# Kernel tuning notes

Measured on AMD Instinct MI355X. Metric: run time of the kernel, lower is better.

The kernel has to match this reference:

```python
import jax, jax.numpy as jnp
import numpy as np
import math

B, S, D, H, FF = 32, 577, 768, 12, 3072
Dh = D // H
EPS = 1e-5


def layer_norm(x, w, b):
    mu = jnp.mean(x, axis=-1, keepdims=True)
    var = jnp.mean(jnp.square(x - mu), axis=-1, keepdims=True)
    return (x - mu) * jax.lax.rsqrt(var + EPS) * w + b


def setup_inputs() -> dict:
    key = jax.random.key(0)
    ks = jax.random.split(key, 12)
    s = 0.02
    return {
        "x": jax.random.normal(ks[0], (B, S, D), dtype=jnp.float32),
        "ln1_w": jnp.ones((D,), jnp.float32),
        "ln1_b": jnp.zeros((D,), jnp.float32),
        # stacked per-head Q/K/V projections (head order matches torch concat order)
        "Wq": jax.random.normal(ks[1], (H, D, Dh), jnp.float32) * s,
        "bq": jnp.zeros((H, Dh), jnp.float32),
        "Wk": jax.random.normal(ks[2], (H, D, Dh), jnp.float32) * s,
        "bk": jnp.zeros((H, Dh), jnp.float32),
        "Wv": jax.random.normal(ks[3], (H, D, Dh), jnp.float32) * s,
        "bv": jnp.zeros((H, Dh), jnp.float32),
        "Wo": jax.random.normal(ks[4], (D, D), jnp.float32) * s,
        "bo": jnp.zeros((D,), jnp.float32),
        "ln2_w": jnp.ones((D,), jnp.float32),
        "ln2_b": jnp.zeros((D,), jnp.float32),
        "W1": jax.random.normal(ks[5], (D, FF), jnp.float32) * s,
        "b1": jnp.zeros((FF,), jnp.float32),
        "W2": jax.random.normal(ks[6], (FF, D), jnp.float32) * s,
        "b2": jnp.zeros((D,), jnp.float32),
    }


def reference(x, ln1_w, ln1_b, Wq, bq, Wk, bk, Wv, bv, Wo, bo, ln2_w, ln2_b, W1, b1, W2, b2):
    # pre-norm attention
    h = layer_norm(x, ln1_w, ln1_b)  # [B,S,D]
    q = jnp.einsum('bsd,hde->bhse', h, Wq) + bq[:, None, :]
    k = jnp.einsum('bsd,hde->bhse', h, Wk) + bk[:, None, :]
    v = jnp.einsum('bsd,hde->bhse', h, Wv) + bv[:, None, :]
    scores = jnp.einsum('bhse,bhte->bhst', q, k) / math.sqrt(Dh)
    probs = jax.nn.softmax(scores, axis=-1)
    ctx = jnp.einsum('bhst,bhte->bhse', probs, v)  # [B,H,S,Dh]
    ctx = ctx.transpose(0, 2, 1, 3).reshape(B, S, H * Dh)  # concat heads
    attn_out = ctx @ Wo + bo
    x = x + attn_out
    # pre-norm MLP (exact GELU, as nn.GELU default)
    h2 = layer_norm(x, ln2_w, ln2_b)
    mlp = jax.nn.gelu(h2 @ W1 + b1, approximate=False) @ W2 + b2
    return x + mlp
```

## Files before the change

### kernel.cpp

```cpp
#include <hip/hip_runtime.h>
#include <hip/hip_bf16.h>
#include <stdint.h>

#define B_ 32
#define S_ 577
#define D_ 768
#define H_ 12
#define FF_ 3072
#define MROWS (B_*S_)

typedef __attribute__((ext_vector_type(8))) short sh8;
typedef __attribute__((ext_vector_type(4))) float f32x4;
typedef __attribute__((ext_vector_type(4))) unsigned short us4;

static __device__ __forceinline__ unsigned short f2b(float f) {
  __hip_bfloat16 h = __float2bfloat16(f);
  return *reinterpret_cast<unsigned short*>(&h);
}
static __device__ __forceinline__ float b2f(unsigned short u) {
  __hip_bfloat16 h;
  *reinterpret_cast<unsigned short*>(&h) = u;
  return __bfloat162float(h);
}

static __device__ __forceinline__ float fast_gelu(float v) {
  const float z = fabsf(v) * 0.70710678118f;
  const float t = __builtin_amdgcn_rcpf(__builtin_fmaf(0.3275911f, z, 1.0f));
  float p = 1.061405429f;
  p = __builtin_fmaf(p, t, -1.453152027f);
  p = __builtin_fmaf(p, t,  1.421413741f);
  p = __builtin_fmaf(p, t, -0.284496736f);
  p = __builtin_fmaf(p, t,  0.254829592f);
  p = p * t;
  const float e = __expf(-z * z);
  const float erf_abs = __builtin_fmaf(-p, e, 1.0f);
  const float erf_v = copysignf(erf_abs, v);
  const float hv = 0.5f * v;
  return __builtin_fmaf(hv, erf_v, hv);
}

#define GLOAD_LDS16(gp, lp) \
  __builtin_amdgcn_global_load_lds((const __attribute__((address_space(1))) unsigned int*)(gp), \
                                   (__attribute__((address_space(3))) unsigned int*)(lp), 16, 0, 0)

__global__ __launch_bounds__(256) void packT64(
    const float* __restrict__ src, unsigned short* __restrict__ dst, int K, int N)
{
  __shared__ unsigned short t[64][65];
  const int tid = threadIdx.x;
  const int c = tid & 63, r4 = tid >> 6;
  const int kb = blockIdx.y * 64, nb = blockIdx.x * 64;
#pragma unroll
  for (int p = 0; p < 16; ++p) {
    const int ko = p * 4 + r4;
    t[c][ko] = f2b(src[(size_t)(kb + ko) * N + nb + c]);
  }
  __syncthreads();
#pragma unroll
  for (int p = 0; p < 16; ++p) {
    const int rr = p * 4 + r4;
    dst[(size_t)(nb + rr) * K + kb + c] = t[rr][c];
  }
}

__global__ __launch_bounds__(256) void packQKV64(
    const float* __restrict__ Wq, const float* __restrict__ Wk, const float* __restrict__ Wv,
    unsigned short* __restrict__ dst)
{
  __shared__ unsigned short t[64][65];
  const int tid = threadIdx.x;
  const int c = tid & 63, r4 = tid >> 6;
  const int kb = blockIdx.x * 64;
  const int h = blockIdx.y;
  const int which = blockIdx.z;
  const float* src = ((which == 0) ? Wq : (which == 1) ? Wk : Wv) + (size_t)h * 768 * 64;
#pragma unroll
  for (int p = 0; p < 16; ++p) {
    const int ko = p * 4 + r4;
    t[c][ko] = f2b(src[(size_t)(kb + ko) * 64 + c]);
  }
  __syncthreads();
  unsigned short* db = dst + (size_t)(which * 768 + h * 64) * 768;
#pragma unroll
  for (int p = 0; p < 16; ++p) {
    const int rr = p * 4 + r4;
    db[(size_t)rr * 768 + kb + c] = t[rr][c];
  }
}

__global__ __launch_bounds__(256) void bias_pack(
    const float* __restrict__ bq, const float* __restrict__ bk, const float* __restrict__ bv,
    float* __restrict__ biasq)
{
  const int idx = blockIdx.x * 256 + threadIdx.x;
  if (idx < 2304) {
    const int wb = idx / 768, rb = idx - wb * 768;
    const float* bb = (wb == 0) ? bq : (wb == 1) ? bk : bv;
    biasq[idx] = bb[rb];
  }
}

__global__ __launch_bounds__(256) void ln_bf16(
    const float* __restrict__ x, const float* __restrict__ w, const float* __restrict__ bse,
    unsigned short* __restrict__ out)
{
  const int row = blockIdx.x;
  const int tid = threadIdx.x;
  const float* xr = x + (size_t)row * 768;
  float v0 = xr[tid], v1 = xr[tid + 256], v2 = xr[tid + 512];
  float s = v0 + v1 + v2;
  float ss = v0 * v0 + v1 * v1 + v2 * v2;
#pragma unroll
  for (int off = 32; off >= 1; off >>= 1) {
    s  += __shfl_xor(s, off);
    ss += __shfl_xor(ss, off);
  }
  __shared__ float red[8];
  const int wv = tid >> 6, ln = tid & 63;
  if (ln == 0) { red[wv] = s; red[wv + 4] = ss; }
  __syncthreads();
  s  = red[0] + red[1] + red[2] + red[3];
  ss = red[4] + red[5] + red[6] + red[7];
  const float mu = s * (1.f / 768.f);
  const float var = ss * (1.f / 768.f) - mu * mu;
  const float rs = rsqrtf(var + 1e-5f);
  unsigned short* orow = out + (size_t)row * 768;
  orow[tid]       = f2b((v0 - mu) * rs * w[tid]       + bse[tid]);
  orow[tid + 256] = f2b((v1 - mu) * rs * w[tid + 256] + bse[tid + 256]);
  orow[tid + 512] = f2b((v2 - mu) * rs * w[tid + 512] + bse[tid + 512]);
}

#define STG_A(t2, dstbase, GRPE) { \
    const int kt2_ = (t2) * 64; \
    _Pragma("unroll") for (int j = 0; j < 2; ++j) { \
      const int idx = wid * 2 + j; \
      const int grp = (GRPE); \
      int grow = bm * 256 + grp * 8 + srow; if (grow >= M) grow = M - 1; \
      GLOAD_LDS16(A + (size_t)grow * K + kt2_ + scol, (dstbase) + grp * 512); \
    } }
#define STG_B(t2, dstbase, GRPE) { \
    const int kt2_ = (t2) * 64; \
    _Pragma("unroll") for (int j = 0; j < 2; ++j) { \
      const int idx = wid * 2 + j; \
      const int grp = (GRPE); \
      const int grow = bn * 256 + grp * 8 + srow; \
      GLOAD_LDS16(Bt + (size_t)grow * K + kt2_ + scol, (dstbase) + grp * 512); \
    } }
#define GRP_A0 (idx + (idx & 8))
#define GRP_A1 (idx + (idx & 8) + 8)
#define GRP_B0 (((idx >> 2) << 3) + (idx & 3))
#define GRP_B1 (((idx >> 2) << 3) + 4 + (idx & 3))
#define LGKM0 asm volatile("s_waitcnt lgkmcnt(0)" ::: "memory"); __builtin_amdgcn_sched_barrier(0)

template<int EPI>
__global__ __launch_bounds__(512, 2) void gemm8p(
    const unsigned short* __restrict__ A, const unsigned short* __restrict__ Bt,
    const float* __restrict__ bias, const float* __restrict__ res,
    unsigned short* __restrict__ obf, float* __restrict__ of32,
    int M, int N, int K)
{
  __shared__ __align__(16) unsigned short sAB[4][256 * 64];
  const int tid = threadIdx.x;
  const int wid = tid >> 6, ln = tid & 63;
  const int wr = wid >> 2, wc = wid & 3;
  const int l15 = ln & 15, lg = ln >> 4;
  const int l7 = l15 & 7;
  const int uo0 = ((lg) ^ l7) * 8;
  const int uo1 = ((4 + lg) ^ l7) * 8;
  const int srow = ln >> 3;
  const int scol = ((ln & 7) ^ srow) * 8;
  const int NT = K >> 6;

  const int nwg = gridDim.x;
  const int gx = N >> 8;
  const int q = nwg >> 3, r = nwg & 7;
  const int x = blockIdx.x & 7, ii = blockIdx.x >> 3;
  const int wg = (x < r ? x * (q + 1) : r * (q + 1) + (x - r) * q) + ii;
  const int bm = wg / gx, bn = wg - bm * gx;

  const int arow = wr * 128 + l15;
  const int brow = wc * 64 + l15;

  f32x4 acc[8][4] = {};
  sh8 afr[4][2], b0r[2][2], b1r[2][2];

  STG_A(0, sAB[0], GRP_A0); STG_A(0, sAB[0], GRP_A1);
  STG_B(0, sAB[2], GRP_B0); STG_B(0, sAB[2], GRP_B1);
  STG_A(1, sAB[1], GRP_A0); STG_A(1, sAB[1], GRP_A1);
  STG_B(1, sAB[3], GRP_B0); STG_B(1, sAB[3], GRP_B1);
  asm volatile("s_waitcnt vmcnt(8)" ::: "memory");
  __builtin_amdgcn_s_barrier();

  for (int t = 0; t < NT; ++t) {
    unsigned short* sAp = sAB[t & 1];
    unsigned short* sBp = sAB[2 + (t & 1)];
    const bool pre = (t + 2 < NT);

#pragma unroll
    for (int mi = 0; mi < 4; ++mi) {
      afr[mi][0] = *(const sh8*)(sAp + (arow + mi * 16) * 64 + uo0);
      afr[mi][1] = *(const sh8*)(sAp + (arow + mi * 16) * 64 + uo1);
    }
#pragma unroll
    for (int ni = 0; ni < 2; ++ni) {
      b0r[ni][0] = *(const sh8*)(sBp + (brow + ni * 16) * 64 + uo0);
      b0r[ni][1] = *(const sh8*)(sBp + (brow + ni * 16) * 64 + uo1);
    }
    __builtin_amdgcn_s_barrier();
    LGKM0;
    __builtin_amdgcn_s_setprio(1);
#pragma unroll
    for (int kk = 0; kk < 2; ++kk)
#pragma unroll
      for (int mi = 0; mi < 4; ++mi)
#pragma unroll
        for (int ni = 0; ni < 2; ++ni)
          acc[mi][ni] = __builtin_amdgcn_mfma_f32_16x16x32_bf16(afr[mi][kk], b0r[ni][kk], acc[mi][ni], 0, 0, 0);
    __builtin_amdgcn_s_setprio(0);
    __builtin_amdgcn_sched_barrier(0);
    __builtin_amdgcn_s_barrier();

#pragma unroll
    for (int ni = 0; ni < 2; ++ni) {
      b1r[ni][0] = *(const sh8*)(sBp + (brow + (ni + 2) * 16) * 64 + uo0);
      b1r[ni][1] = *(const sh8*)(sBp + (brow + (ni + 2) * 16) * 64 + uo1);
    }
    if (pre) STG_A(t + 2, sAp, GRP_A0);
    __builtin_amdgcn_s_barrier();
    LGKM0;
    __builtin_amdgcn_s_setprio(1);
#pragma unroll
    for (int kk = 0; kk < 2; ++kk)
#pragma unroll
      for (int mi = 0; mi < 4; ++mi)
#pragma unroll
        for (int ni = 0; ni < 2; ++ni)
          acc[mi][ni + 2] = __builtin_amdgcn_mfma_f32_16x16x32_bf16(afr[mi][kk], b1r[ni][kk], acc[mi][ni + 2], 0, 0, 0);
    __builtin_amdgcn_s_setprio(0);
    __builtin_amdgcn_sched_barrier(0);
    __builtin_amdgcn_s_barrier();

#pragma unroll
    for (int mi = 0; mi < 4; ++mi) {
      afr[mi][0] = *(const sh8*)(sAp + (arow + (mi + 4) * 16) * 64 + uo0);
      afr[mi][1] = *(const sh8*)(sAp + (arow + (mi + 4) * 16) * 64 + uo1);
    }
    if (pre) { STG_B(t + 2, sBp, GRP_B0); STG_B(t + 2, sBp, GRP_B1); }
    __builtin_amdgcn_s_barrier();
    LGKM0;
    __builtin_amdgcn_s_setprio(1);
#pragma unroll
    for (int kk = 0; kk < 2; ++kk)
#pragma unroll
      for (int mi = 0; mi < 4; ++mi)
#pragma unroll
        for (int ni = 0; ni < 2; ++ni)
          acc[mi + 4][ni + 2] = __builtin_amdgcn_mfma_f32_16x16x32_bf16(afr[mi][kk], b1r[ni][kk], acc[mi + 4][ni + 2], 0, 0, 0);
    __builtin_amdgcn_s_setprio(0);
    __builtin_amdgcn_sched_barrier(0);
    __builtin_amdgcn_s_barrier();

    if (pre) STG_A(t + 2, sAp, GRP_A1);
    __builtin_amdgcn_s_barrier();
    __builtin_amdgcn_s_setprio(1);
#pragma unroll
    for (int kk = 0; kk < 2; ++kk)
#pragma unroll
      for (int mi = 0; mi < 4; ++mi)
#pragma unroll
        for (int ni = 0; ni < 2; ++ni)
          acc[mi + 4][ni] = __builtin_amdgcn_mfma_f32_16x16x32_bf16(afr[mi][kk], b0r[ni][kk], acc[mi + 4][ni], 0, 0, 0);
    __builtin_amdgcn_s_setprio(0);
    __builtin_amdgcn_sched_barrier(0);
    if (t + 1 < NT) {
      if (pre) { asm volatile("s_waitcnt vmcnt(8)" ::: "memory"); }
      else     { asm volatile("s_waitcnt vmcnt(0)" ::: "memory"); }
      __builtin_amdgcn_s_barrier();
    }
  }

  constexpr int ESTR = 260;
  float* eps = (float*)sAB;
#pragma unroll
  for (int pass = 0; pass < 4; ++pass) {
    __builtin_amdgcn_s_barrier();
    if (wr == (pass >> 1)) {
      const int mib = (pass & 1) * 4;
#pragma unroll
      for (int mi = 0; mi < 4; ++mi)
#pragma unroll
        for (int ni = 0; ni < 4; ++ni)
#pragma unroll
          for (int rr = 0; rr < 4; ++rr)
            eps[(mi * 16 + lg * 4 + rr) * ESTR + wc * 64 + ni * 16 + l15] = acc[mib + mi][ni][rr];
    }
    __builtin_amdgcn_s_barrier();
#pragma unroll
    for (int p = 0; p < 8; ++p) {
      const int idx = p * 512 + tid;
      const int rl = idx >> 6;
      const int c4 = (idx & 63) * 4;
      const int grow = bm * 256 + pass * 64 + rl;
      if (grow < M) {
        f32x4 v = *(const f32x4*)(eps + rl * ESTR + c4);
        const int gcol = bn * 256 + c4;
        const f32x4 bv = *(const f32x4*)(bias + gcol);
        v += bv;
        if (EPI == 2) {
#pragma unroll
          for (int e = 0; e < 4; ++e) v[e] = fast_gelu(v[e]);
        }
        if (EPI == 1) {
          const f32x4 rv = *(const f32x4*)(res + (size_t)grow * N + gcol);
          v += rv;
          *(f32x4*)(of32 + (size_t)grow * N + gcol) = v;
        } else {
          us4 o = { f2b(v[0]), f2b(v[1]), f2b(v[2]), f2b(v[3]) };
          *(us4*)(obf + (size_t)grow * N + gcol) = o;
        }
      }
    }
  }
}

__global__ __launch_bounds__(256) void attn(
    const unsigned short* __restrict__ qkv, unsigned short* __restrict__ ctx)
{
  constexpr int KP = 72;
  __shared__ __align__(16) unsigned short sQ[64 * KP];
  __shared__ __align__(16) unsigned short sK[64 * KP];
  __shared__ __align__(16) unsigned short sVT[64 * KP];
  __shared__ __align__(16) unsigned short sP[4][16 * KP];
  const int tid = threadIdx.x, wv = tid >> 6, ln = tid & 63;
  const int l15 = ln & 15, lg = ln >> 4;
  const int b = blockIdx.z, h = blockIdx.y, qt = blockIdx.x;
  const size_t base = (size_t)b * S_ * 2304 + h * 64;
  const unsigned short* qp = qkv + base;
  const unsigned short* kp = qkv + base + 768;
  const unsigned short* vp = qkv + base + 1536;

  {
    const int r = tid >> 2, c = (tid & 3) * 16;
    int row = qt * 64 + r; if (row >= S_) row = S_ - 1;
    const unsigned short* g = qp + (size_t)row * 2304 + c;
#pragma unroll
    for (int half = 0; half < 2; ++half) {
      sh8 v = *(const sh8*)(g + half * 8);
      unsigned short o[8];
#pragma unroll
      for (int j = 0; j < 8; ++j) o[j] = f2b(b2f((unsigned short)v[j]) * 0.125f);
      *(sh8*)(sQ + r * KP + c + half * 8) = *(sh8*)o;
    }
  }

  f32x4 oacc[4] = {};
  float m_run = -1e30f, l_run = 0.f;
  const int nt = (S_ + 63) / 64;
  for (int t = 0; t < nt; ++t) {
    __syncthreads();
    {
      const int r = tid >> 2, c = (tid & 3) * 16;
      int row = t * 64 + r; if (row >= S_) row = S_ - 1;
      const unsigned short* g = kp + (size_t)row * 2304 + c;
      *(sh8*)(sK + r * KP + c)     = *(const sh8*)g;
      *(sh8*)(sK + r * KP + c + 8) = *(const sh8*)(g + 8);
    }
#pragma unroll
    for (int uu = 0; uu < 2; ++uu) {
      const int u = tid + uu * 256;
      const int e = u & 63, kvb = u >> 6;
      unsigned short val[8];
#pragma unroll
      for (int j = 0; j < 8; ++j) {
        int row = t * 64 + kvb * 8 + j; if (row >= S_) row = S_ - 1;
        val[j] = vp[(size_t)row * 2304 + e];
      }
      *(sh8*)(sVT + e * KP + kvb * 8) = *(sh8*)val;
    }
    __syncthreads();

    f32x4 sacc[4] = {};
#pragma unroll
    for (int kk = 0; kk < 2; ++kk) {
      sh8 bq = *(const sh8*)(sQ + (wv * 16 + l15) * KP + kk * 32 + lg * 8);
#pragma unroll
      for (int f = 0; f < 4; ++f) {
        sh8 ak = *(const sh8*)(sK + (f * 16 + l15) * KP + kk * 32 + lg * 8);
        sacc[f] = __builtin_amdgcn_mfma_f32_16x16x32_bf16(ak, bq, sacc[f], 0, 0, 0);
      }
    }

    float sv[4][4];
    float pmax = -1e30f;
#pragma unroll
    for (int f = 0; f < 4; ++f)
#pragma unroll
      for (int r = 0; r < 4; ++r) {
        const int kva = t * 64 + f * 16 + lg * 4 + r;
        float sc = sacc[f][r];
        if (kva >= S_) sc = -1e30f;
        sv[f][r] = sc;
        pmax = fmaxf(pmax, sc);
      }
    pmax = fmaxf(pmax, __shfl_xor(pmax, 16));
    pmax = fmaxf(pmax, __shfl_xor(pmax, 32));
    const float mnew = fmaxf(m_run, pmax);
    const float alpha = __expf(m_run - mnew);
    float psum = 0.f;
    unsigned short pb[4][4];
#pragma unroll
    for (int f = 0; f < 4; ++f)
#pragma unroll
      for (int r = 0; r < 4; ++r) {
        const float p = __expf(sv[f][r] - mnew);
        psum += p;
        pb[f][r] = f2b(p);
      }
    psum += __shfl_xor(psum, 16);
    psum += __shfl_xor(psum, 32);
    l_run = l_run * alpha + psum;
    m_run = mnew;
#pragma unroll
    for (int f = 0; f < 4; ++f) {
      oacc[f][0] *= alpha; oacc[f][1] *= alpha;
      oacc[f][2] *= alpha; oacc[f][3] *= alpha;
    }
#pragma unroll
    for (int f = 0; f < 4; ++f) {
      us4 pk = { pb[f][0], pb[f][1], pb[f][2], pb[f][3] };
      *(us4*)(sP[wv] + l15 * KP + f * 16 + lg * 4) = pk;
    }
    __syncthreads();

#pragma unroll
    for (int kk = 0; kk < 2; ++kk) {
      sh8 bp = *(const sh8*)(sP[wv] + l15 * KP + kk * 32 + lg * 8);
#pragma unroll
      for (int fe = 0; fe < 4; ++fe) {
        sh8 av = *(const sh8*)(sVT + (fe * 16 + l15) * KP + kk * 32 + lg * 8);
        oacc[fe] = __builtin_amdgcn_mfma_f32_16x16x32_bf16(av, bp, oacc[fe], 0, 0, 0);
      }
    }
  }

  const int qa = qt * 64 + wv * 16 + l15;
  if (qa < S_) {
    const float inv = 1.f / l_run;
    const size_t orow = ((size_t)b * S_ + qa) * 768 + h * 64;
#pragma unroll
    for (int fe = 0; fe < 4; ++fe) {
      unsigned short pk[4];
#pragma unroll
      for (int r = 0; r < 4; ++r) pk[r] = f2b(oacc[fe][r] * inv);
      *(us4*)(ctx + orow + fe * 16 + lg * 4) = *(us4*)pk;
    }
  }
}

extern "C" void kernel_launch(void* const* d_in, const int* in_sizes, int n_in,
                              void* d_out, int out_size, void* d_ws, size_t ws_size,
                              hipStream_t stream)
{
  const float* x    = (const float*)d_in[0];
  const float* ln1w = (const float*)d_in[1];
  const float* ln1b = (const float*)d_in[2];
  const float* Wq   = (const float*)d_in[3];
  const float* bq   = (const float*)d_in[4];
  const float* Wk   = (const float*)d_in[5];
  const float* bk   = (const float*)d_in[6];
  const float* Wv   = (const float*)d_in[7];
  const float* bv   = (const float*)d_in[8];
  const float* Wo   = (const float*)d_in[9];
  const float* bo   = (const float*)d_in[10];
  const float* ln2w = (const float*)d_in[11];
  const float* ln2b = (const float*)d_in[12];
  const float* W1   = (const float*)d_in[13];
  const float* b1   = (const float*)d_in[14];
  const float* W2   = (const float*)d_in[15];
  const float* b2   = (const float*)d_in[16];
  float* out = (float*)d_out;
  char* ws = (char*)d_ws;

  unsigned short* wqkvT = (unsigned short*)(ws + 0);
  unsigned short* woT   = (unsigned short*)(ws + 3538944);
  unsigned short* w1T   = (unsigned short*)(ws + 4718592);
  unsigned short* w2T   = (unsigned short*)(ws + 9437184);
  float*          biasq = (float*)(ws + 14155776);
  unsigned short* hbf   = (unsigned short*)(ws + 14164992);
  unsigned short* qkvb  = (unsigned short*)(ws + 42525696);
  unsigned short* ctxb  = (unsigned short*)(ws + 127607808);
  unsigned short* mlp1  = qkvb;

  packQKV64<<<dim3(12, 12, 3), 256, 0, stream>>>(Wq, Wk, Wv, wqkvT);
  bias_pack<<<9, 256, 0, stream>>>(bq, bk, bv, biasq);
  packT64<<<dim3(12, 12), 256, 0, stream>>>(Wo, woT, 768, 768);
  packT64<<<dim3(48, 12), 256, 0, stream>>>(W1, w1T, 768, 3072);
  packT64<<<dim3(12, 48), 256, 0, stream>>>(W2, w2T, 3072, 768);

  ln_bf16<<<MROWS, 256, 0, stream>>>(x, ln1w, ln1b, hbf);
  gemm8p<0><<<9 * 73, 512, 0, stream>>>(hbf, wqkvT, biasq, nullptr, qkvb, nullptr,
                                        MROWS, 2304, 768);
  attn<<<dim3(10, 12, 32), 256, 0, stream>>>(qkvb, ctxb);
  gemm8p<1><<<3 * 73, 512, 0, stream>>>(ctxb, woT, bo, x, nullptr, out,
                                        MROWS, 768, 768);
  ln_bf16<<<MROWS, 256, 0, stream>>>(out, ln2w, ln2b, hbf);
  gemm8p<2><<<12 * 73, 512, 0, stream>>>(hbf, w1T, b1, nullptr, mlp1, nullptr,
                                         MROWS, 3072, 768);
  gemm8p<1><<<3 * 73, 512, 0, stream>>>(mlp1, w2T, b2, out, nullptr, out,
                                        MROWS, 768, 3072);
}
```

Before: 522.1 us.

## Make GEMM persistent with 256 workgroups and overlap next-tile prefetch with epilogue

The GEMM kernel now launches a fixed grid of 256 workgroups. Each one walks a contiguous range of output tiles, with blocks spread across XCDs by interleaving. While the epilogue of the current tile runs, the A operand of the next tile is prefetched into the A buffers. The epilogue now stages results through the B half of shared memory in eight 32-row passes so it does not clash with that prefetch. The goal is to cut the tail effect from partial waves and hide the load latency at tile boundaries, at the cost of more complex synchronisation and possible load imbalance when tile counts don't divide evenly.

Measured after the change: 531.9 us. No clear change (+1.9%).

```diff
diff --git a/kernel.cpp b/kernel.cpp
--- a/kernel.cpp
+++ b/kernel.cpp
@@ -171,155 +171,176 @@
   const int scol = ((ln & 7) ^ srow) * 8;
   const int NT = K >> 6;
 
-  const int nwg = gridDim.x;
   const int gx = N >> 8;
-  const int q = nwg >> 3, r = nwg & 7;
-  const int x = blockIdx.x & 7, ii = blockIdx.x >> 3;
-  const int wg = (x < r ? x * (q + 1) : r * (q + 1) + (x - r) * q) + ii;
-  const int bm = wg / gx, bn = wg - bm * gx;
+  const int tiles = ((M + 255) >> 8) * gx;
+  const int p = (blockIdx.x & 7) * 32 + (blockIdx.x >> 3);
+  const int q = tiles >> 8, r = tiles & 255;
+  int tt = p * q + (p < r ? p : r);
+  const int tend = tt + q + (p < r ? 1 : 0);
+  if (tt >= tend) return;
+
+  int bm = tt / gx, bn = tt - bm * gx;
 
   const int arow = wr * 128 + l15;
   const int brow = wc * 64 + l15;
 
-  f32x4 acc[8][4] = {};
   sh8 afr[4][2], b0r[2][2], b1r[2][2];
 
   STG_A(0, sAB[0], GRP_A0); STG_A(0, sAB[0], GRP_A1);
+  STG_A(1, sAB[1], GRP_A0); STG_A(1, sAB[1], GRP_A1);
   STG_B(0, sAB[2], GRP_B0); STG_B(0, sAB[2], GRP_B1);
-  STG_A(1, sAB[1], GRP_A0); STG_A(1, sAB[1], GRP_A1);
   STG_B(1, sAB[3], GRP_B0); STG_B(1, sAB[3], GRP_B1);
-  asm volatile("s_waitcnt vmcnt(8)" ::: "memory");
+  asm volatile("s_waitcnt vmcnt(4)" ::: "memory");
   __builtin_amdgcn_s_barrier();
 
-  for (int t = 0; t < NT; ++t) {
-    unsigned short* sAp = sAB[t & 1];
-    unsigned short* sBp = sAB[2 + (t & 1)];
-    const bool pre = (t + 2 < NT);
-
-#pragma unroll
-    for (int mi = 0; mi < 4; ++mi) {
-      afr[mi][0] = *(const sh8*)(sAp + (arow + mi * 16) * 64 + uo0);
-      afr[mi][1] = *(const sh8*)(sAp + (arow + mi * 16) * 64 + uo1);
-    }
-#pragma unroll
-    for (int ni = 0; ni < 2; ++ni) {
-      b0r[ni][0] = *(const sh8*)(sBp + (brow + ni * 16) * 64 + uo0);
-      b0r[ni][1] = *(const sh8*)(sBp + (brow + ni * 16) * 64 + uo1);
-    }
+  while (true) {
+    f32x4 acc[8][4] = {};
+
+    for (int t = 0; t < NT; ++t) {
+      unsigned short* sAp = sAB[t & 1];
+      unsigned short* sBp = sAB[2 + (t & 1)];
+      const bool pre = (t + 2 < NT);
+
+#pragma unroll
+      for (int mi = 0; mi < 4; ++mi) {
+        afr[mi][0] = *(const sh8*)(sAp + (arow + mi * 16) * 64 + uo0);
+        afr[mi][1] = *(const sh8*)(sAp + (arow + mi * 16) * 64 + uo1);
+      }
+#pragma unroll
+      for (int ni = 0; ni < 2; ++ni) {
+        b0r[ni][0] = *(const sh8*)(sBp + (brow + ni * 16) * 64 + uo0);
+        b0r[ni][1] = *(const sh8*)(sBp + (brow + ni * 16) * 64 + uo1);
+        b1r[ni][0] = *(const sh8*)(sBp + (brow + (ni + 2) * 16) * 64 + uo0);
+        b1r[ni][1] = *(const sh8*)(sBp + (brow + (ni + 2) * 16) * 64 + uo1);
+      }
+      __builtin_amdgcn_s_barrier();
+      LGKM0;
+      __builtin_amdgcn_s_setprio(1);
+#pragma unroll
+      for (int kk = 0; kk < 2; ++kk)
+#pragma unroll
+        for (int mi = 0; mi < 4; ++mi)
+#pragma unroll
+          for (int ni = 0; ni < 2; ++ni)
+            acc[mi][ni] = __builtin_amdgcn_mfma_f32_16x16x32_bf16(afr[mi][kk], b0r[ni][kk], acc[mi][ni], 0, 0, 0);
+      __builtin_amdgcn_s_setprio(0);
+      __builtin_amdgcn_sched_barrier(0);
+      __builtin_amdgcn_s_barrier();
+
+      if (pre) STG_A(t + 2, sAp, GRP_A0);
+      __builtin_amdgcn_s_barrier();
+      LGKM0;
+      __builtin_amdgcn_s_setprio(1);
+#pragma unroll
+      for (int kk = 0; kk < 2; ++kk)
+#pragma unroll
+        for (int mi = 0; mi < 4; ++mi)
+#pragma unroll
+          for (int ni = 0; ni < 2; ++ni)
+            acc[mi][ni + 2] = __builtin_amdgcn_mfma_f32_16x16x32_bf16(afr[mi][kk], b1r[ni][kk], acc[mi][ni + 2], 0, 0, 0);
+      __builtin_amdgcn_s_setprio(0);
+      __builtin_amdgcn_sched_barrier(0);
+      __builtin_amdgcn_s_barrier();
+
+#pragma unroll
+      for (int mi = 0; mi < 4; ++mi) {
+        afr[mi][0] = *(const sh8*)(sAp + (arow + (mi + 4) * 16) * 64 + uo0);
+        afr[mi][1] = *(const sh8*)(sAp + (arow + (mi + 4) * 16) * 64 + uo1);
+      }
+      if (pre) { STG_B(t + 2, sBp, GRP_B0); STG_B(t + 2, sBp, GRP_B1); }
+      __builtin_amdgcn_s_barrier();
+      LGKM0;
+      __builtin_amdgcn_s_setprio(1);
+#pragma unroll
+      for (int kk = 0; kk < 2; ++kk)
+#pragma unroll
+        for (int mi = 0; mi < 4; ++mi)
+#pragma unroll
+          for (int ni = 0; ni < 2; ++ni)
+            acc[mi + 4][ni + 2] = __builtin_amdgcn_mfma_f32_16x16x32_bf16(afr[mi][kk], b1r[ni][kk], acc[mi + 4][ni + 2], 0, 0, 0);
+      __builtin_amdgcn_s_setprio(0);
+      __builtin_amdgcn_sched_barrier(0);
+      __builtin_amdgcn_s_barrier();
+
+      if (pre) STG_A(t + 2, sAp, GRP_A1);
+      __builtin_amdgcn_s_barrier();
+      __builtin_amdgcn_s_setprio(1);
+#pragma unroll
+      for (int kk = 0; kk < 2; ++kk)
+#pragma unroll
+        for (int mi = 0; mi < 4; ++mi)
+#pragma unroll
+          for (int ni = 0; ni < 2; ++ni)
+            acc[mi + 4][ni] = __builtin_amdgcn_mfma_f32_16x16x32_bf16(afr[mi][kk], b0r[ni][kk], acc[mi + 4][ni], 0, 0, 0);
+      __builtin_amdgcn_s_setprio(0);
+      __builtin_amdgcn_sched_barrier(0);
+      if (t + 1 < NT) {
+        if (pre) { asm volatile("s_waitcnt vmcnt(8)" ::: "memory"); }
+        else     { asm volatile("s_waitcnt vmcnt(0)" ::: "memory"); }
+        __builtin_amdgcn_s_barrier();
+      }
+    }
+
+    const int obm = bm, obn = bn;
+    const bool more = (tt + 1 < tend);
+    if (more) { ++tt; bm = tt / gx; bn = tt - bm * gx; }
+
     __builtin_amdgcn_s_barrier();
-    LGKM0;
-    __builtin_amdgcn_s_setprio(1);
-#pragma unroll
-    for (int kk = 0; kk < 2; ++kk)
-#pragma unroll
-      for (int mi = 0; mi < 4; ++mi)
-#pragma unroll
-        for (int ni = 0; ni < 2; ++ni)
-          acc[mi][ni] = __builtin_amdgcn_mfma_f32_16x16x32_bf16(afr[mi][kk], b0r[ni][kk], acc[mi][ni], 0, 0, 0);
-    __builtin_amdgcn_s_setprio(0);
-    __builtin_amdgcn_sched_barrier(0);
+    if (more) {
+      STG_A(0, sAB[0], GRP_A0); STG_A(0, sAB[0], GRP_A1);
+      STG_A(1, sAB[1], GRP_A0); STG_A(1, sAB[1], GRP_A1);
+    }
+
+    constexpr int ESTR = 260;
+    float* eps = (float*)(sAB[2]);
+#pragma unroll
+    for (int pass = 0; pass < 8; ++pass) {
+      __builtin_amdgcn_s_barrier();
+      if (wr == (pass >> 2)) {
+        const int mib = (pass & 3) * 2;
+#pragma unroll
+        for (int mi = 0; mi < 2; ++mi)
+#pragma unroll
+          for (int ni = 0; ni < 4; ++ni)
+#pragma unroll
+            for (int rr = 0; rr < 4; ++rr)
+              eps[(mi * 16 + lg * 4 + rr) * ESTR + wc * 64 + ni * 16 + l15] = acc[mib + mi][ni][rr];
+      }
+      __builtin_amdgcn_s_barrier();
+#pragma unroll
+      for (int pp = 0; pp < 4; ++pp) {
+        const int idx = pp * 512 + tid;
+        const int rl = idx >> 6;
+        const int c4 = (idx & 63) * 4;
+        const int grow = obm * 256 + pass * 32 + rl;
+        if (grow < M) {
+          f32x4 v = *(const f32x4*)(eps + rl * ESTR + c4);
+          const int gcol = obn * 256 + c4;
+          const f32x4 bv = *(const f32x4*)(bias + gcol);
+          v += bv;
+          if (EPI == 2) {
+#pragma unroll
+            for (int e = 0; e < 4; ++e) v[e] = fast_gelu(v[e]);
+          }
+          if (EPI == 1) {
+            const f32x4 rv = *(const f32x4*)(res + (size_t)grow * N + gcol);
+            v += rv;
+            *(f32x4*)(of32 + (size_t)grow * N + gcol) = v;
+          } else {
+            us4 o = { f2b(v[0]), f2b(v[1]), f2b(v[2]), f2b(v[3]) };
+            *(us4*)(obf + (size_t)grow * N + gcol) = o;
+          }
+        }
+      }
+    }
+
+    if (!more) break;
+
     __builtin_amdgcn_s_barrier();
-
-#pragma unroll
-    for (int ni = 0; ni < 2; ++ni) {
-      b1r[ni][0] = *(const sh8*)(sBp + (brow + (ni + 2) * 16) * 64 + uo0);
-      b1r[ni][1] = *(const sh8*)(sBp + (brow + (ni + 2) * 16) * 64 + uo1);
-    }
-    if (pre) STG_A(t + 2, sAp, GRP_A0);
+    STG_B(0, sAB[2], GRP_B0); STG_B(0, sAB[2], GRP_B1);
+    STG_B(1, sAB[3], GRP_B0); STG_B(1, sAB[3], GRP_B1);
+    asm volatile("s_waitcnt vmcnt(4)" ::: "memory");
     __builtin_amdgcn_s_barrier();
-    LGKM0;
-    __builtin_amdgcn_s_setprio(1);
-#pragma unroll
-    for (int kk = 0; kk < 2; ++kk)
-#pragma unroll
-      for (int mi = 0; mi < 4; ++mi)
-#pragma unroll
-        for (int ni = 0; ni < 2; ++ni)
-          acc[mi][ni + 2] = __builtin_amdgcn_mfma_f32_16x16x32_bf16(afr[mi][kk], b1r[ni][kk], acc[mi][ni + 2], 0, 0, 0);
-    __builtin_amdgcn_s_setprio(0);
-    __builtin_amdgcn_sched_barrier(0);
-    __builtin_amdgcn_s_barrier();
-
-#pragma unroll
-    for (int mi = 0; mi < 4; ++mi) {
-      afr[mi][0] = *(const sh8*)(sAp + (arow + (mi + 4) * 16) * 64 + uo0);
-      afr[mi][1] = *(const sh8*)(sAp + (arow + (mi + 4) * 16) * 64 + uo1);
-    }
-    if (pre) { STG_B(t + 2, sBp, GRP_B0); STG_B(t + 2, sBp, GRP_B1); }
-    __builtin_amdgcn_s_barrier();
-    LGKM0;
-    __builtin_amdgcn_s_setprio(1);
-#pragma unroll
-    for (int kk = 0; kk < 2; ++kk)
-#pragma unroll
-      for (int mi = 0; mi < 4; ++mi)
-#pragma unroll
-        for (int ni = 0; ni < 2; ++ni)
-          acc[mi + 4][ni + 2] = __builtin_amdgcn_mfma_f32_16x16x32_bf16(afr[mi][kk], b1r[ni][kk], acc[mi + 4][ni + 2], 0, 0, 0);
-    __builtin_amdgcn_s_setprio(0);
-    __builtin_amdgcn_sched_barrier(0);
-    __builtin_amdgcn_s_barrier();
-
-    if (pre) STG_A(t + 2, sAp, GRP_A1);
-    __builtin_amdgcn_s_barrier();
-    __builtin_amdgcn_s_setprio(1);
-#pragma unroll
-    for (int kk = 0; kk < 2; ++kk)
-#pragma unroll
-      for (int mi = 0; mi < 4; ++mi)
-#pragma unroll
-        for (int ni = 0; ni < 2; ++ni)
-          acc[mi + 4][ni] = __builtin_amdgcn_mfma_f32_16x16x32_bf16(afr[mi][kk], b0r[ni][kk], acc[mi + 4][ni], 0, 0, 0);
-    __builtin_amdgcn_s_setprio(0);
-    __builtin_amdgcn_sched_barrier(0);
-    if (t + 1 < NT) {
-      if (pre) { asm volatile("s_waitcnt vmcnt(8)" ::: "memory"); }
-      else     { asm volatile("s_waitcnt vmcnt(0)" ::: "memory"); }
-      __builtin_amdgcn_s_barrier();
-    }
-  }
-
-  constexpr int ESTR = 260;
-  float* eps = (float*)sAB;
-#pragma unroll
-  for (int pass = 0; pass < 4; ++pass) {
-    __builtin_amdgcn_s_barrier();
-    if (wr == (pass >> 1)) {
-      const int mib = (pass & 1) * 4;
-#pragma unroll
-      for (int mi = 0; mi < 4; ++mi)
-#pragma unroll
-        for (int ni = 0; ni < 4; ++ni)
-#pragma unroll
-          for (int rr = 0; rr < 4; ++rr)
-            eps[(mi * 16 + lg * 4 + rr) * ESTR + wc * 64 + ni * 16 + l15] = acc[mib + mi][ni][rr];
-    }
-    __builtin_amdgcn_s_barrier();
-#pragma unroll
-    for (int p = 0; p < 8; ++p) {
-      const int idx = p * 512 + tid;
-      const int rl = idx >> 6;
-      const int c4 = (idx & 63) * 4;
-      const int grow = bm * 256 + pass * 64 + rl;
-      if (grow < M) {
-        f32x4 v = *(const f32x4*)(eps + rl * ESTR + c4);
-        const int gcol = bn * 256 + c4;
-        const f32x4 bv = *(const f32x4*)(bias + gcol);
-        v += bv;
-        if (EPI == 2) {
-#pragma unroll
-          for (int e = 0; e < 4; ++e) v[e] = fast_gelu(v[e]);
-        }
-        if (EPI == 1) {
-          const f32x4 rv = *(const f32x4*)(res + (size_t)grow * N + gcol);
-          v += rv;
-          *(f32x4*)(of32 + (size_t)grow * N + gcol) = v;
-        } else {
-          us4 o = { f2b(v[0]), f2b(v[1]), f2b(v[2]), f2b(v[3]) };
-          *(us4*)(obf + (size_t)grow * N + gcol) = o;
-        }
-      }
-    }
   }
 }
 
@@ -498,14 +519,14 @@
   packT64<<<dim3(12, 48), 256, 0, stream>>>(W2, w2T, 3072, 768);
 
   ln_bf16<<<MROWS, 256, 0, stream>>>(x, ln1w, ln1b, hbf);
-  gemm8p<0><<<9 * 73, 512, 0, stream>>>(hbf, wqkvT, biasq, nullptr, qkvb, nullptr,
-                                        MROWS, 2304, 768);
+  gemm8p<0><<<256, 512, 0, stream>>>(hbf, wqkvT, biasq, nullptr, qkvb, nullptr,
+                                     MROWS, 2304, 768);
   attn<<<dim3(10, 12, 32), 256, 0, stream>>>(qkvb, ctxb);
-  gemm8p<1><<<3 * 73, 512, 0, stream>>>(ctxb, woT, bo, x, nullptr, out,
-                                        MROWS, 768, 768);
+  gemm8p<1><<<256, 512, 0, stream>>>(ctxb, woT, bo, x, nullptr, out,
+                                     MROWS, 768, 768);
   ln_bf16<<<MROWS, 256, 0, stream>>>(out, ln2w, ln2b, hbf);
-  gemm8p<2><<<12 * 73, 512, 0, stream>>>(hbf, w1T, b1, nullptr, mlp1, nullptr,
-                                         MROWS, 3072, 768);
-  gemm8p<1><<<3 * 73, 512, 0, stream>>>(mlp1, w2T, b2, out, nullptr, out,
-                                        MROWS, 768, 3072);
-}
+  gemm8p<2><<<256, 512, 0, stream>>>(hbf, w1T, b1, nullptr, mlp1, nullptr,
+                                     MROWS, 3072, 768);
+  gemm8p<1><<<256, 512, 0, stream>>>(mlp1, w2T, b2, out, nullptr, out,
+                                     MROWS, 768, 3072);
+}
```

## Replace 256x256 pipelined GEMM with simpler 128x128 single-buffered GEMM

Applied to the files above, without the earlier changes.

Swaps the 512-thread 256x256-tile GEMM, which double-buffers LDS and interleaves its prefetches with the MFMA phases, for a 256-thread 128x128-tile kernel. The new kernel loads each K-step into a single LDS buffer, waits on vmcnt(0), syncs, and then runs the MFMAs. The aim is higher occupancy (3 blocks per CU) and a finer grid that balances better across CUs. In exchange it loses global-load/compute overlap and halves per-tile data reuse, adding more global traffic and synchronisation stalls.

Result: faster. 493.8 us (-5.4%).

```diff
diff --git a/kernel.cpp b/kernel.cpp
--- a/kernel.cpp
+++ b/kernel.cpp
@@ -130,39 +130,17 @@
   orow[tid + 512] = f2b((v2 - mu) * rs * w[tid + 512] + bse[tid + 512]);
 }
 
-#define STG_A(t2, dstbase, GRPE) { \
-    const int kt2_ = (t2) * 64; \
-    _Pragma("unroll") for (int j = 0; j < 2; ++j) { \
-      const int idx = wid * 2 + j; \
-      const int grp = (GRPE); \
-      int grow = bm * 256 + grp * 8 + srow; if (grow >= M) grow = M - 1; \
-      GLOAD_LDS16(A + (size_t)grow * K + kt2_ + scol, (dstbase) + grp * 512); \
-    } }
-#define STG_B(t2, dstbase, GRPE) { \
-    const int kt2_ = (t2) * 64; \
-    _Pragma("unroll") for (int j = 0; j < 2; ++j) { \
-      const int idx = wid * 2 + j; \
-      const int grp = (GRPE); \
-      const int grow = bn * 256 + grp * 8 + srow; \
-      GLOAD_LDS16(Bt + (size_t)grow * K + kt2_ + scol, (dstbase) + grp * 512); \
-    } }
-#define GRP_A0 (idx + (idx & 8))
-#define GRP_A1 (idx + (idx & 8) + 8)
-#define GRP_B0 (((idx >> 2) << 3) + (idx & 3))
-#define GRP_B1 (((idx >> 2) << 3) + 4 + (idx & 3))
-#define LGKM0 asm volatile("s_waitcnt lgkmcnt(0)" ::: "memory"); __builtin_amdgcn_sched_barrier(0)
-
 template<int EPI>
-__global__ __launch_bounds__(512, 2) void gemm8p(
+__global__ __launch_bounds__(256, 3) void gemm128(
     const unsigned short* __restrict__ A, const unsigned short* __restrict__ Bt,
     const float* __restrict__ bias, const float* __restrict__ res,
     unsigned short* __restrict__ obf, float* __restrict__ of32,
     int M, int N, int K)
 {
-  __shared__ __align__(16) unsigned short sAB[4][256 * 64];
+  __shared__ __align__(16) unsigned short sAB[2][128 * 64];
   const int tid = threadIdx.x;
   const int wid = tid >> 6, ln = tid & 63;
-  const int wr = wid >> 2, wc = wid & 3;
+  const int wr = wid >> 1, wc = wid & 1;
   const int l15 = ln & 15, lg = ln >> 4;
   const int l7 = l15 & 7;
   const int uo0 = ((lg) ^ l7) * 8;
@@ -171,139 +149,79 @@
   const int scol = ((ln & 7) ^ srow) * 8;
   const int NT = K >> 6;
 
+  const int gx = N >> 7;
   const int nwg = gridDim.x;
-  const int gx = N >> 8;
   const int q = nwg >> 3, r = nwg & 7;
   const int x = blockIdx.x & 7, ii = blockIdx.x >> 3;
   const int wg = (x < r ? x * (q + 1) : r * (q + 1) + (x - r) * q) + ii;
   const int bm = wg / gx, bn = wg - bm * gx;
 
-  const int arow = wr * 128 + l15;
+  const int arow = wr * 64 + l15;
   const int brow = wc * 64 + l15;
 
-  f32x4 acc[8][4] = {};
-  sh8 afr[4][2], b0r[2][2], b1r[2][2];
-
-  STG_A(0, sAB[0], GRP_A0); STG_A(0, sAB[0], GRP_A1);
-  STG_B(0, sAB[2], GRP_B0); STG_B(0, sAB[2], GRP_B1);
-  STG_A(1, sAB[1], GRP_A0); STG_A(1, sAB[1], GRP_A1);
-  STG_B(1, sAB[3], GRP_B0); STG_B(1, sAB[3], GRP_B1);
-  asm volatile("s_waitcnt vmcnt(8)" ::: "memory");
-  __builtin_amdgcn_s_barrier();
+  f32x4 acc[4][4] = {};
 
   for (int t = 0; t < NT; ++t) {
-    unsigned short* sAp = sAB[t & 1];
-    unsigned short* sBp = sAB[2 + (t & 1)];
-    const bool pre = (t + 2 < NT);
-
-#pragma unroll
-    for (int mi = 0; mi < 4; ++mi) {
-      afr[mi][0] = *(const sh8*)(sAp + (arow + mi * 16) * 64 + uo0);
-      afr[mi][1] = *(const sh8*)(sAp + (arow + mi * 16) * 64 + uo1);
-    }
-#pragma unroll
-    for (int ni = 0; ni < 2; ++ni) {
-      b0r[ni][0] = *(const sh8*)(sBp + (brow + ni * 16) * 64 + uo0);
-      b0r[ni][1] = *(const sh8*)(sBp + (brow + ni * 16) * 64 + uo1);
-    }
-    __builtin_amdgcn_s_barrier();
-    LGKM0;
-    __builtin_amdgcn_s_setprio(1);
-#pragma unroll
-    for (int kk = 0; kk < 2; ++kk)
+    const int kt = t * 64;
+    __syncthreads();
+#pragma unroll
+    for (int j = 0; j < 4; ++j) {
+      const int idx = wid * 4 + j;
+      int ga = bm * 128 + idx * 8 + srow; if (ga >= M) ga = M - 1;
+      GLOAD_LDS16(A + (size_t)ga * K + kt + scol, sAB[0] + idx * 512);
+    }
+#pragma unroll
+    for (int j = 0; j < 4; ++j) {
+      const int idx = wid * 4 + j;
+      const int gb = bn * 128 + idx * 8 + srow;
+      GLOAD_LDS16(Bt + (size_t)gb * K + kt + scol, sAB[1] + idx * 512);
+    }
+    asm volatile("s_waitcnt vmcnt(0)" ::: "memory");
+    __syncthreads();
+
+#pragma unroll
+    for (int kk = 0; kk < 2; ++kk) {
+      const int uo = kk ? uo1 : uo0;
+      sh8 af[4], bf[4];
 #pragma unroll
       for (int mi = 0; mi < 4; ++mi)
-#pragma unroll
-        for (int ni = 0; ni < 2; ++ni)
-          acc[mi][ni] = __builtin_amdgcn_mfma_f32_16x16x32_bf16(afr[mi][kk], b0r[ni][kk], acc[mi][ni], 0, 0, 0);
-    __builtin_amdgcn_s_setprio(0);
-    __builtin_amdgcn_sched_barrier(0);
-    __builtin_amdgcn_s_barrier();
-
-#pragma unroll
-    for (int ni = 0; ni < 2; ++ni) {
-      b1r[ni][0] = *(const sh8*)(sBp + (brow + (ni + 2) * 16) * 64 + uo0);
-      b1r[ni][1] = *(const sh8*)(sBp + (brow + (ni + 2) * 16) * 64 + uo1);
-    }
-    if (pre) STG_A(t + 2, sAp, GRP_A0);
-    __builtin_amdgcn_s_barrier();
-    LGKM0;
-    __builtin_amdgcn_s_setprio(1);
-#pragma unroll
-    for (int kk = 0; kk < 2; ++kk)
+        af[mi] = *(const sh8*)(sAB[0] + (arow + mi * 16) * 64 + uo);
+#pragma unroll
+      for (int ni = 0; ni < 4; ++ni)
+        bf[ni] = *(const sh8*)(sAB[1] + (brow + ni * 16) * 64 + uo);
 #pragma unroll
       for (int mi = 0; mi < 4; ++mi)
 #pragma unroll
-        for (int ni = 0; ni < 2; ++ni)
-          acc[mi][ni + 2] = __builtin_amdgcn_mfma_f32_16x16x32_bf16(afr[mi][kk], b1r[ni][kk], acc[mi][ni + 2], 0, 0, 0);
-    __builtin_amdgcn_s_setprio(0);
-    __builtin_amdgcn_sched_barrier(0);
-    __builtin_amdgcn_s_barrier();
-
-#pragma unroll
-    for (int mi = 0; mi < 4; ++mi) {
-      afr[mi][0] = *(const sh8*)(sAp + (arow + (mi + 4) * 16) * 64 + uo0);
-      afr[mi][1] = *(const sh8*)(sAp + (arow + (mi + 4) * 16) * 64 + uo1);
-    }
-    if (pre) { STG_B(t + 2, sBp, GRP_B0); STG_B(t + 2, sBp, GRP_B1); }
-    __builtin_amdgcn_s_barrier();
-    LGKM0;
-    __builtin_amdgcn_s_setprio(1);
-#pragma unroll
-    for (int kk = 0; kk < 2; ++kk)
-#pragma unroll
-      for (int mi = 0; mi < 4; ++mi)
-#pragma unroll
-        for (int ni = 0; ni < 2; ++ni)
-          acc[mi + 4][ni + 2] = __builtin_amdgcn_mfma_f32_16x16x32_bf16(afr[mi][kk], b1r[ni][kk], acc[mi + 4][ni + 2], 0, 0, 0);
-    __builtin_amdgcn_s_setprio(0);
-    __builtin_amdgcn_sched_barrier(0);
-    __builtin_amdgcn_s_barrier();
-
-    if (pre) STG_A(t + 2, sAp, GRP_A1);
-    __builtin_amdgcn_s_barrier();
-    __builtin_amdgcn_s_setprio(1);
-#pragma unroll
-    for (int kk = 0; kk < 2; ++kk)
-#pragma unroll
-      for (int mi = 0; mi < 4; ++mi)
-#pragma unroll
-        for (int ni = 0; ni < 2; ++ni)
-          acc[mi + 4][ni] = __builtin_amdgcn_mfma_f32_16x16x32_bf16(afr[mi][kk], b0r[ni][kk], acc[mi + 4][ni], 0, 0, 0);
-    __builtin_amdgcn_s_setprio(0);
-    __builtin_amdgcn_sched_barrier(0);
-    if (t + 1 < NT) {
-      if (pre) { asm volatile("s_waitcnt vmcnt(8)" ::: "memory"); }
-      else     { asm volatile("s_waitcnt vmcnt(0)" ::: "memory"); }
-      __builtin_amdgcn_s_barrier();
-    }
-  }
-
-  constexpr int ESTR = 260;
+        for (int ni = 0; ni < 4; ++ni)
+          acc[mi][ni] = __builtin_amdgcn_mfma_f32_16x16x32_bf16(af[mi], bf[ni], acc[mi][ni], 0, 0, 0);
+    }
+  }
+
+  constexpr int ESTR = 132;
   float* eps = (float*)sAB;
 #pragma unroll
   for (int pass = 0; pass < 4; ++pass) {
-    __builtin_amdgcn_s_barrier();
+    __syncthreads();
     if (wr == (pass >> 1)) {
-      const int mib = (pass & 1) * 4;
-#pragma unroll
-      for (int mi = 0; mi < 4; ++mi)
+      const int mib = (pass & 1) * 2;
+#pragma unroll
+      for (int ml = 0; ml < 2; ++ml)
 #pragma unroll
         for (int ni = 0; ni < 4; ++ni)
 #pragma unroll
           for (int rr = 0; rr < 4; ++rr)
-            eps[(mi * 16 + lg * 4 + rr) * ESTR + wc * 64 + ni * 16 + l15] = acc[mib + mi][ni][rr];
-    }
-    __builtin_amdgcn_s_barrier();
-#pragma unroll
-    for (int p = 0; p < 8; ++p) {
-      const int idx = p * 512 + tid;
-      const int rl = idx >> 6;
-      const int c4 = (idx & 63) * 4;
-      const int grow = bm * 256 + pass * 64 + rl;
+            eps[(ml * 16 + lg * 4 + rr) * ESTR + wc * 64 + ni * 16 + l15] = acc[mib + ml][ni][rr];
+    }
+    __syncthreads();
+#pragma unroll
+    for (int pp = 0; pp < 4; ++pp) {
+      const int idx = pp * 256 + tid;
+      const int rl = idx >> 5;
+      const int c4 = (idx & 31) * 4;
+      const int grow = bm * 128 + pass * 32 + rl;
       if (grow < M) {
         f32x4 v = *(const f32x4*)(eps + rl * ESTR + c4);
-        const int gcol = bn * 256 + c4;
+        const int gcol = bn * 128 + c4;
         const f32x4 bv = *(const f32x4*)(bias + gcol);
         v += bv;
         if (EPI == 2) {
@@ -498,14 +416,14 @@
   packT64<<<dim3(12, 48), 256, 0, stream>>>(W2, w2T, 3072, 768);
 
   ln_bf16<<<MROWS, 256, 0, stream>>>(x, ln1w, ln1b, hbf);
-  gemm8p<0><<<9 * 73, 512, 0, stream>>>(hbf, wqkvT, biasq, nullptr, qkvb, nullptr,
-                                        MROWS, 2304, 768);
+  gemm128<0><<<145 * 18, 256, 0, stream>>>(hbf, wqkvT, biasq, nullptr, qkvb, nullptr,
+                                           MROWS, 2304, 768);
   attn<<<dim3(10, 12, 32), 256, 0, stream>>>(qkvb, ctxb);
-  gemm8p<1><<<3 * 73, 512, 0, stream>>>(ctxb, woT, bo, x, nullptr, out,
-                                        MROWS, 768, 768);
+  gemm128<1><<<145 * 6, 256, 0, stream>>>(ctxb, woT, bo, x, nullptr, out,
+                                          MROWS, 768, 768);
   ln_bf16<<<MROWS, 256, 0, stream>>>(out, ln2w, ln2b, hbf);
-  gemm8p<2><<<12 * 73, 512, 0, stream>>>(hbf, w1T, b1, nullptr, mlp1, nullptr,
-                                         MROWS, 3072, 768);
-  gemm8p<1><<<3 * 73, 512, 0, stream>>>(mlp1, w2T, b2, out, nullptr, out,
-                                        MROWS, 768, 3072);
-}
+  gemm128<2><<<145 * 24, 256, 0, stream>>>(hbf, w1T, b1, nullptr, mlp1, nullptr,
+                                           MROWS, 3072, 768);
+  gemm128<1><<<145 * 6, 256, 0, stream>>>(mlp1, w2T, b2, out, nullptr, out,
+                                          MROWS, 768, 3072);
+}
```
